# Kernel optimization log

Measured on AMD Instinct MI355X. Metric: run time of the kernel, lower is better.

The kernel has to match this reference:

```python
import jax, jax.numpy as jnp
import numpy as np


def _graph_conv(feat_src, e_src, e_dst, n_src, n_dst, W, b):
    # DGL GraphConv, norm='both', bipartite block; feat_src: [N_src, A, C, H]
    ones_e = jnp.ones(e_src.shape[0], dtype=feat_src.dtype)
    out_deg = jax.ops.segment_sum(ones_e, e_src, num_segments=n_src)
    in_deg = jax.ops.segment_sum(ones_e, e_dst, num_segments=n_dst)
    norm_src = jnp.clip(out_deg, 1.0) ** -0.5
    norm_dst = jnp.clip(in_deg, 1.0) ** -0.5
    feat = feat_src * norm_src[:, None, None, None]
    # in_feats == out_feats -> DGL multiplies by W before aggregation
    feat = jnp.einsum('nach,ho->naco', feat, W)
    msgs = feat[e_src]                                   # gather  [E, A, C, H]
    agg = jax.ops.segment_sum(msgs, e_dst, num_segments=n_dst)  # scatter-add
    return agg * norm_dst[:, None, None, None] + b


def setup_inputs() -> dict:
    key = jax.random.key(0)
    ks = jax.random.split(key, 8)
    H = 128
    N_SRC0, N_DST0, N_DST1 = 50000, 20000, 4096
    E0, E1 = 320000, 65536
    return {
        'in_feat': jax.random.normal(ks[0], (2, H, 2, N_SRC0), dtype=jnp.float32),
        'W': jax.random.normal(ks[1], (H, H), dtype=jnp.float32) / np.sqrt(H),
        'b': jnp.zeros((H,), dtype=jnp.float32),
        'e0_src': jax.random.randint(ks[2], (E0,), 0, N_SRC0, dtype=jnp.int32),
        'e0_dst': jax.random.randint(ks[3], (E0,), 0, N_DST0, dtype=jnp.int32),
        'e1_src': jax.random.randint(ks[4], (E1,), 0, N_DST0, dtype=jnp.int32),
        'e1_dst': jax.random.randint(ks[5], (E1,), 0, N_DST1, dtype=jnp.int32),
        'n_dst0': N_DST0,
        'n_dst1': N_DST1,
    }


def reference(in_feat, W, b, e0_src, e0_dst, e1_src, e1_dst, n_dst0, n_dst1):
    # [A, H, C, N] -> [N, A, C, H]
    x = jnp.transpose(in_feat, (3, 0, 2, 1))
    n_src0 = x.shape[0]
    h = _graph_conv(x, e0_src, e0_dst, n_src0, n_dst0, W, b)
    h = jax.nn.relu(h)
    h = _graph_conv(h, e1_src, e1_dst, n_dst0, n_dst1, W, b)
    h = jax.nn.relu(h)
    # [N_dst1, A, C, H] -> [A, H, C, N_dst1]
    out = jnp.transpose(h, (1, 3, 2, 0))
    return jax.nn.relu(out)
```

## Files before the change

kernel.cpp:

```cpp
#include <hip/hip_runtime.h>
#include <math.h>

#define H128 128
#define NF 512
typedef unsigned short u16;
typedef __attribute__((ext_vector_type(8))) short short8;
typedef __attribute__((ext_vector_type(4))) float floatx4;

__device__ inline u16 f2bf(float f) {
  union { float f; unsigned u; } x; x.f = f;
  unsigned r = x.u + 0x7FFFu + ((x.u >> 16) & 1u);
  return (u16)(r >> 16);
}
__device__ inline void addbf8(float* a, uint4 u) {
  a[0] += __uint_as_float(u.x << 16);
  a[1] += __uint_as_float(u.x & 0xFFFF0000u);
  a[2] += __uint_as_float(u.y << 16);
  a[3] += __uint_as_float(u.y & 0xFFFF0000u);
  a[4] += __uint_as_float(u.z << 16);
  a[5] += __uint_as_float(u.z & 0xFFFF0000u);
  a[6] += __uint_as_float(u.w << 16);
  a[7] += __uint_as_float(u.w & 0xFFFF0000u);
}

__global__ void k_count4(const int* __restrict__ e0s, const int* __restrict__ e0d,
                         const int* __restrict__ e1s, const int* __restrict__ e1d,
                         int E0, int E1,
                         int* __restrict__ c_s0, int* __restrict__ c_d0,
                         int* __restrict__ c_s1, int* __restrict__ c_d1) {
  int i = blockIdx.x * 256 + threadIdx.x;
  if (i < E0) { atomicAdd(&c_s0[e0s[i]], 1); return; }
  i -= E0;
  if (i < E0) { atomicAdd(&c_d0[e0d[i]], 1); return; }
  i -= E0;
  if (i < E1) { atomicAdd(&c_s1[e1s[i]], 1); return; }
  i -= E1;
  if (i < E1) { atomicAdd(&c_d1[e1d[i]], 1); }
}

__global__ void k_norm(int* __restrict__ buf, int n) {
  int i = blockIdx.x * 256 + threadIdx.x;
  if (i < n) {
    int d = buf[i];
    float dv = (d < 1) ? 1.0f : (float)d;
    ((float*)buf)[i] = 1.0f / sqrtf(dv);
  }
}

__global__ void k_scan2(const int* __restrict__ degA, int nA, int* __restrict__ offA, int* __restrict__ curA,
                        const int* __restrict__ degB, int nB, int* __restrict__ offB, int* __restrict__ curB) {
  const int* deg = blockIdx.x ? degB : degA;
  int n = blockIdx.x ? nB : nA;
  int* off = blockIdx.x ? offB : offA;
  int* cur = blockIdx.x ? curB : curA;
  __shared__ int wsum[16];
  const int tid = threadIdx.x;
  const int lane = tid & 63;
  const int wv = tid >> 6;
  const int per = (n + 1023) >> 10;
  const int base = tid * per;
  int cnt = n - base;
  if (cnt < 0) cnt = 0;
  if (cnt > per) cnt = per;
  int sum = 0;
  for (int i = 0; i < cnt; ++i) sum += deg[base + i];
  int x = sum;
  #pragma unroll
  for (int d2 = 1; d2 < 64; d2 <<= 1) {
    int y = __shfl_up(x, (unsigned)d2, 64);
    if (lane >= d2) x += y;
  }
  if (lane == 63) wsum[wv] = x;
  __syncthreads();
  if (wv == 0 && lane < 16) {
    int w = wsum[lane];
    #pragma unroll
    for (int d2 = 1; d2 < 16; d2 <<= 1) {
      int y = __shfl_up(w, (unsigned)d2, 64);
      if (lane >= d2) w += y;
    }
    wsum[lane] = w;
  }
  __syncthreads();
  int tbase = x - sum + (wv ? wsum[wv - 1] : 0);
  int running = tbase;
  for (int i = 0; i < cnt; ++i) {
    off[base + i] = running;
    cur[base + i] = running;
    running += deg[base + i];
  }
  if (tid == 1023) off[n] = wsum[15];
}

__global__ void k_scatter2(const int* __restrict__ e0s, const int* __restrict__ e0d,
                           const int* __restrict__ e1s, const int* __restrict__ e1d,
                           int E0, int E1,
                           int* __restrict__ cur0, int* __restrict__ csr0,
                           int* __restrict__ cur1, int* __restrict__ csr1) {
  int i = blockIdx.x * 256 + threadIdx.x;
  if (i < E0) {
    int p = atomicAdd(&cur0[e0d[i]], 1);
    csr0[p] = e0s[i];
    return;
  }
  i -= E0;
  if (i < E1) {
    int p = atomicAdd(&cur1[e1d[i]], 1);
    csr1[p] = e1s[i];
  }
}

__global__ void k_wfrag(const float* __restrict__ W, uint4* __restrict__ wfrag) {
  int t = blockIdx.x * 256 + threadIdx.x;
  int lane = t & 63;
  int pair = t >> 6;
  int ct = pair >> 2, kc = pair & 3;
  int quad = lane >> 4, r = lane & 15;
  const float* src = W + (size_t)(kc * 32 + quad * 8) * 128 + ct * 16 + r;
  union { u16 v[8]; uint4 u; } pk;
  #pragma unroll
  for (int j = 0; j < 8; ++j) pk.v[j] = f2bf(src[(size_t)j * 128]);
  wfrag[t] = pk.u;
}

__global__ __launch_bounds__(256) void k_transpose_in(
    const float* __restrict__ in, const float* __restrict__ norm,
    u16* __restrict__ xp, int N) {
  __shared__ float tile[64 * 128];
  const int tid = threadIdx.x;
  const int n0 = blockIdx.x << 6;
  const int ac = blockIdx.y;
  const int a = ac >> 1, c = ac & 1;
  const float* base = in + ((size_t)a * 256 + c) * (size_t)N;
  #pragma unroll
  for (int i = 0; i < 8; ++i) {
    int fidx = (i << 8) + tid;
    int h = fidx >> 4;
    int t = fidx & 15;
    int n = t << 2;
    int gn = n0 + n;
    float4 v = make_float4(0.f, 0.f, 0.f, 0.f);
    if (gn < N) v = *(const float4*)(base + (size_t)h * 2 * N + gn);
    int q = h >> 2, rem = h & 3;
    int rot = ((q + t) & 31) << 2;
    tile[(n + 0) * 128 + rot + rem] = v.x;
    tile[(n + 1) * 128 + rot + rem] = v.y;
    tile[(n + 2) * 128 + rot + rem] = v.z;
    tile[(n + 3) * 128 + rot + rem] = v.w;
  }
  __syncthreads();
  #pragma unroll
  for (int i = 0; i < 8; ++i) {
    int fidx = (i << 8) + tid;
    int h4 = fidx & 31;
    int n = fidx >> 5;
    int gn = n0 + n;
    if (gn < N) {
      float4 v = *(const float4*)(&tile[n * 128 + (((h4 + (n >> 2)) & 31) << 2)]);
      float s = norm[gn];
      ushort4 o;
      o.x = f2bf(v.x * s); o.y = f2bf(v.y * s);
      o.z = f2bf(v.z * s); o.w = f2bf(v.w * s);
      *(ushort4*)(xp + (size_t)gn * NF + ac * H128 + (h4 << 2)) = o;
    }
  }
}

__global__ __launch_bounds__(256) void k_agg(
    const u16* __restrict__ xp, const int* __restrict__ csr,
    const int* __restrict__ off, const float* __restrict__ norm_dst,
    u16* __restrict__ outp, int ndst) {
  const int wave = threadIdx.x >> 6;
  const int lane = threadIdx.x & 63;
  const int d = blockIdx.x * 4 + wave;
  if (d >= ndst) return;
  const int s = off[d], e = off[d + 1];
  float acc[8];
  #pragma unroll
  for (int i = 0; i < 8; ++i) acc[i] = 0.f;
  int j = s;
  for (; j + 4 <= e; j += 4) {
    int s0 = csr[j], s1 = csr[j + 1], s2 = csr[j + 2], s3 = csr[j + 3];
    uint4 u0 = *((const uint4*)(xp + (size_t)s0 * NF) + lane);
    uint4 u1 = *((const uint4*)(xp + (size_t)s1 * NF) + lane);
    uint4 u2 = *((const uint4*)(xp + (size_t)s2 * NF) + lane);
    uint4 u3 = *((const uint4*)(xp + (size_t)s3 * NF) + lane);
    addbf8(acc, u0); addbf8(acc, u1); addbf8(acc, u2); addbf8(acc, u3);
  }
  for (; j < e; ++j) {
    uint4 u = *((const uint4*)(xp + (size_t)csr[j] * NF) + lane);
    addbf8(acc, u);
  }
  float nd = norm_dst[d];
  u16* orow = outp + (size_t)d * NF + lane * 8;
  ushort4 o0, o1;
  o0.x = f2bf(acc[0] * nd); o0.y = f2bf(acc[1] * nd);
  o0.z = f2bf(acc[2] * nd); o0.w = f2bf(acc[3] * nd);
  o1.x = f2bf(acc[4] * nd); o1.y = f2bf(acc[5] * nd);
  o1.z = f2bf(acc[6] * nd); o1.w = f2bf(acc[7] * nd);
  *(ushort4*)orow = o0;
  *(ushort4*)(orow + 4) = o1;
}

template <bool OUT_BF16>
__global__ __launch_bounds__(256) void k_gemm_mfma(
    const u16* __restrict__ A, const uint4* __restrict__ wfrag,
    const float* __restrict__ bias, const float* __restrict__ scale,
    void* __restrict__ outv, int M) {
  __shared__ uint4 wb[2048];
  const int tid = threadIdx.x;
  #pragma unroll
  for (int i = 0; i < 8; ++i) wb[i * 256 + tid] = wfrag[i * 256 + tid];
  __syncthreads();
  const int wave = tid >> 6;
  const int lane = tid & 63;
  const int quad = lane >> 4;
  const int r = lane & 15;
  const int row0 = (blockIdx.x * 4 + wave) << 4;
  if (row0 >= M) return;
  short8 a[4];
  const u16* abase = A + (size_t)(row0 + r) * 128 + quad * 8;
  #pragma unroll
  for (int kc = 0; kc < 4; ++kc) a[kc] = *(const short8*)(abase + kc * 32);
  floatx4 acc[8];
  #pragma unroll
  for (int ct = 0; ct < 8; ++ct) acc[ct] = (floatx4){0.f, 0.f, 0.f, 0.f};
  #pragma unroll
  for (int kc = 0; kc < 4; ++kc) {
    #pragma unroll
    for (int ct = 0; ct < 8; ++ct) {
      short8 b = *(const short8*)&wb[(ct * 4 + kc) * 64 + lane];
      acc[ct] = __builtin_amdgcn_mfma_f32_16x16x32_bf16(a[kc], b, acc[ct], 0, 0, 0);
    }
  }
  float sc = scale ? scale[(row0 >> 2) + quad] : 1.f;
  #pragma unroll
  for (int ct = 0; ct < 8; ++ct) {
    float bcol = bias[ct * 16 + r];
    #pragma unroll
    for (int reg = 0; reg < 4; ++reg) {
      float v = acc[ct][reg] + bcol;
      v = (v > 0.f ? v : 0.f) * sc;
      size_t idx = (size_t)(row0 + quad * 4 + reg) * 128 + ct * 16 + r;
      if (OUT_BF16) ((u16*)outv)[idx] = f2bf(v);
      else          ((float*)outv)[idx] = v;
    }
  }
}

__global__ __launch_bounds__(256) void k_transpose_out(
    const float* __restrict__ h1, float* __restrict__ out, int N) {
  __shared__ float tile[128][68];
  const int tid = threadIdx.x;
  const int n0 = blockIdx.x << 6;
  const int ac = blockIdx.y;
  const int a = ac >> 1, c = ac & 1;
  #pragma unroll
  for (int i = 0; i < 8; ++i) {
    int fidx = (i << 8) + tid;
    int h4 = fidx & 31;
    int n = fidx >> 5;
    float4 v = *(const float4*)(h1 + (size_t)(n0 + n) * NF + ac * H128 + (h4 << 2));
    int h = h4 << 2;
    tile[h + 0][n] = v.x; tile[h + 1][n] = v.y;
    tile[h + 2][n] = v.z; tile[h + 3][n] = v.w;
  }
  __syncthreads();
  float* obase = out + ((size_t)a * 256 + c) * (size_t)N;
  #pragma unroll
  for (int i = 0; i < 8; ++i) {
    int fidx = (i << 8) + tid;
    int h = fidx >> 4;
    int n = (fidx & 15) << 2;
    float4 v = *(const float4*)(&tile[h][n]);
    *(float4*)(obase + (size_t)h * 2 * N + n0 + n) = v;
  }
}

extern "C" void kernel_launch(void* const* d_in, const int* in_sizes, int n_in,
                              void* d_out, int out_size, void* d_ws, size_t ws_size,
                              hipStream_t stream) {
  const float* in_feat = (const float*)d_in[0];
  const float* W       = (const float*)d_in[1];
  const float* bias    = (const float*)d_in[2];
  const int* e0_src    = (const int*)d_in[3];
  const int* e0_dst    = (const int*)d_in[4];
  const int* e1_src    = (const int*)d_in[5];
  const int* e1_dst    = (const int*)d_in[6];
  const int N_DST0 = 20000;
  const int N_DST1 = 4096;
  const int N_SRC0 = in_sizes[0] / NF;
  const int E0 = in_sizes[3];
  const int E1 = in_sizes[5];

  u16* xp    = (u16*)d_ws;
  u16* h0    = xp + (size_t)N_SRC0 * NF;
  u16* agg0b = h0 + (size_t)N_DST0 * NF;
  u16* agg1b = agg0b + (size_t)N_DST0 * NF;
  float* h1  = (float*)(agg1b + (size_t)N_DST1 * NF);
  int* ibase    = (int*)(h1 + (size_t)N_DST1 * NF);
  int* cnt_src0 = ibase;
  int* cnt_dst0 = cnt_src0 + N_SRC0;
  int* cnt_src1 = cnt_dst0 + N_DST0;
  int* cnt_dst1 = cnt_src1 + N_DST0;
  int* off0 = cnt_dst1 + N_DST1;
  int* cur0 = off0 + N_DST0 + 1;
  int* csr0 = cur0 + N_DST0;
  int* off1 = csr0 + E0;
  int* cur1 = off1 + N_DST1 + 1;
  int* csr1 = cur1 + N_DST1;
  uint4* wfrag = (uint4*)(((uintptr_t)(csr1 + E1) + 15) & ~(uintptr_t)15);

  const int NCNT = N_SRC0 + N_DST0 + N_DST0 + N_DST1;
  hipMemsetAsync(cnt_src0, 0, (size_t)NCNT * sizeof(int), stream);

  int tot_cnt = 2 * E0 + 2 * E1;
  k_count4<<<(tot_cnt + 255) / 256, 256, 0, stream>>>(
      e0_src, e0_dst, e1_src, e1_dst, E0, E1, cnt_src0, cnt_dst0, cnt_src1, cnt_dst1);

  k_scan2<<<2, 1024, 0, stream>>>(cnt_dst0, N_DST0, off0, cur0,
                                  cnt_dst1, N_DST1, off1, cur1);

  k_norm<<<(NCNT + 255) / 256, 256, 0, stream>>>(cnt_src0, NCNT);

  k_scatter2<<<(E0 + E1 + 255) / 256, 256, 0, stream>>>(
      e0_src, e0_dst, e1_src, e1_dst, E0, E1, cur0, csr0, cur1, csr1);

  k_wfrag<<<8, 256, 0, stream>>>(W, wfrag);

  dim3 tg1((N_SRC0 + 63) / 64, 4);
  k_transpose_in<<<tg1, 256, 0, stream>>>(in_feat, (const float*)cnt_src0, xp, N_SRC0);

  k_agg<<<(N_DST0 + 3) / 4, 256, 0, stream>>>(
      xp, csr0, off0, (const float*)cnt_dst0, agg0b, N_DST0);
  k_gemm_mfma<true><<<(N_DST0 * 4) / 64, 256, 0, stream>>>(
      agg0b, wfrag, bias, (const float*)cnt_src1, (void*)h0, N_DST0 * 4);

  k_agg<<<(N_DST1 + 3) / 4, 256, 0, stream>>>(
      h0, csr1, off1, (const float*)cnt_dst1, agg1b, N_DST1);
  k_gemm_mfma<false><<<(N_DST1 * 4) / 64, 256, 0, stream>>>(
      agg1b, wfrag, bias, nullptr, (void*)h1, N_DST1 * 4);

  dim3 tg2(N_DST1 / 64, 4);
  k_transpose_out<<<tg2, 256, 0, stream>>>(h1, (float*)d_out, N_DST1);
}
```

Baseline: 354.8 us.

## Merge preprocessing kernels and fuse CSR scatter with input transpose

Folds count4 into a two-atomic-per-thread count kernel, merges scan, norm and weight-fragment conversion into one multi-role prep kernel, and runs the CSR scatter in the same launch as the input transpose by partitioning blocks. Degree norms now go to a separate float buffer so the scan and the norm computation can run concurrently. The aggregation loop is unrolled to 8 outstanding gathers to raise memory-level parallelism. Together these cut the number of launches and the serialization between small kernels, at the cost of role-divergent blocks and a larger transpose block size.

Result: faster. 338.8 us (-4.5%).

```diff
diff --git a/kernel.cpp b/kernel.cpp
--- a/kernel.cpp
+++ b/kernel.cpp
@@ -23,118 +23,130 @@
   a[7] += __uint_as_float(u.w & 0xFFFF0000u);
 }
 
-__global__ void k_count4(const int* __restrict__ e0s, const int* __restrict__ e0d,
+__global__ void k_count2(const int* __restrict__ e0s, const int* __restrict__ e0d,
                          const int* __restrict__ e1s, const int* __restrict__ e1d,
                          int E0, int E1,
                          int* __restrict__ c_s0, int* __restrict__ c_d0,
                          int* __restrict__ c_s1, int* __restrict__ c_d1) {
   int i = blockIdx.x * 256 + threadIdx.x;
-  if (i < E0) { atomicAdd(&c_s0[e0s[i]], 1); return; }
-  i -= E0;
-  if (i < E0) { atomicAdd(&c_d0[e0d[i]], 1); return; }
-  i -= E0;
-  if (i < E1) { atomicAdd(&c_s1[e1s[i]], 1); return; }
-  i -= E1;
-  if (i < E1) { atomicAdd(&c_d1[e1d[i]], 1); }
-}
-
-__global__ void k_norm(int* __restrict__ buf, int n) {
-  int i = blockIdx.x * 256 + threadIdx.x;
-  if (i < n) {
-    int d = buf[i];
-    float dv = (d < 1) ? 1.0f : (float)d;
-    ((float*)buf)[i] = 1.0f / sqrtf(dv);
-  }
-}
-
-__global__ void k_scan2(const int* __restrict__ degA, int nA, int* __restrict__ offA, int* __restrict__ curA,
-                        const int* __restrict__ degB, int nB, int* __restrict__ offB, int* __restrict__ curB) {
-  const int* deg = blockIdx.x ? degB : degA;
-  int n = blockIdx.x ? nB : nA;
-  int* off = blockIdx.x ? offB : offA;
-  int* cur = blockIdx.x ? curB : curA;
-  __shared__ int wsum[16];
-  const int tid = threadIdx.x;
-  const int lane = tid & 63;
-  const int wv = tid >> 6;
-  const int per = (n + 1023) >> 10;
-  const int base = tid * per;
-  int cnt = n - base;
-  if (cnt < 0) cnt = 0;
-  if (cnt > per) cnt = per;
-  int sum = 0;
-  for (int i = 0; i < cnt; ++i) sum += deg[base + i];
-  int x = sum;
-  #pragma unroll
-  for (int d2 = 1; d2 < 64; d2 <<= 1) {
-    int y = __shfl_up(x, (unsigned)d2, 64);
-    if (lane >= d2) x += y;
-  }
-  if (lane == 63) wsum[wv] = x;
-  __syncthreads();
-  if (wv == 0 && lane < 16) {
-    int w = wsum[lane];
-    #pragma unroll
-    for (int d2 = 1; d2 < 16; d2 <<= 1) {
-      int y = __shfl_up(w, (unsigned)d2, 64);
-      if (lane >= d2) w += y;
-    }
-    wsum[lane] = w;
-  }
-  __syncthreads();
-  int tbase = x - sum + (wv ? wsum[wv - 1] : 0);
-  int running = tbase;
-  for (int i = 0; i < cnt; ++i) {
-    off[base + i] = running;
-    cur[base + i] = running;
-    running += deg[base + i];
-  }
-  if (tid == 1023) off[n] = wsum[15];
-}
-
-__global__ void k_scatter2(const int* __restrict__ e0s, const int* __restrict__ e0d,
-                           const int* __restrict__ e1s, const int* __restrict__ e1d,
-                           int E0, int E1,
-                           int* __restrict__ cur0, int* __restrict__ csr0,
-                           int* __restrict__ cur1, int* __restrict__ csr1) {
-  int i = blockIdx.x * 256 + threadIdx.x;
   if (i < E0) {
-    int p = atomicAdd(&cur0[e0d[i]], 1);
-    csr0[p] = e0s[i];
+    atomicAdd(&c_s0[e0s[i]], 1);
+    atomicAdd(&c_d0[e0d[i]], 1);
     return;
   }
   i -= E0;
   if (i < E1) {
-    int p = atomicAdd(&cur1[e1d[i]], 1);
-    csr1[p] = e1s[i];
-  }
-}
-
-__global__ void k_wfrag(const float* __restrict__ W, uint4* __restrict__ wfrag) {
-  int t = blockIdx.x * 256 + threadIdx.x;
-  int lane = t & 63;
-  int pair = t >> 6;
-  int ct = pair >> 2, kc = pair & 3;
-  int quad = lane >> 4, r = lane & 15;
-  const float* src = W + (size_t)(kc * 32 + quad * 8) * 128 + ct * 16 + r;
-  union { u16 v[8]; uint4 u; } pk;
-  #pragma unroll
-  for (int j = 0; j < 8; ++j) pk.v[j] = f2bf(src[(size_t)j * 128]);
-  wfrag[t] = pk.u;
-}
-
-__global__ __launch_bounds__(256) void k_transpose_in(
+    atomicAdd(&c_s1[e1s[i]], 1);
+    atomicAdd(&c_d1[e1d[i]], 1);
+  }
+}
+
+__global__ __launch_bounds__(1024) void k_prep(
+    const int* __restrict__ cnt, int NCNT, float* __restrict__ normf,
+    const int* __restrict__ degA, int nA, int* __restrict__ offA, int* __restrict__ curA,
+    const int* __restrict__ degB, int nB, int* __restrict__ offB, int* __restrict__ curB,
+    const float* __restrict__ W, uint4* __restrict__ wfrag) {
+  __shared__ int wsum[16];
+  const int b = blockIdx.x;
+  const int tid = threadIdx.x;
+  if (b < 2) {
+    const int* deg = b ? degB : degA;
+    int n = b ? nB : nA;
+    int* off = b ? offB : offA;
+    int* cur = b ? curB : curA;
+    const int lane = tid & 63;
+    const int wv = tid >> 6;
+    const int per = (n + 1023) >> 10;
+    const int base = tid * per;
+    int cntk = n - base;
+    if (cntk < 0) cntk = 0;
+    if (cntk > per) cntk = per;
+    int sum = 0;
+    for (int i = 0; i < cntk; ++i) sum += deg[base + i];
+    int x = sum;
+    #pragma unroll
+    for (int d2 = 1; d2 < 64; d2 <<= 1) {
+      int y = __shfl_up(x, (unsigned)d2, 64);
+      if (lane >= d2) x += y;
+    }
+    if (lane == 63) wsum[wv] = x;
+    __syncthreads();
+    if (wv == 0 && lane < 16) {
+      int w = wsum[lane];
+      #pragma unroll
+      for (int d2 = 1; d2 < 16; d2 <<= 1) {
+        int y = __shfl_up(w, (unsigned)d2, 64);
+        if (lane >= d2) w += y;
+      }
+      wsum[lane] = w;
+    }
+    __syncthreads();
+    int tbase = x - sum + (wv ? wsum[wv - 1] : 0);
+    int running = tbase;
+    for (int i = 0; i < cntk; ++i) {
+      off[base + i] = running;
+      cur[base + i] = running;
+      running += deg[base + i];
+    }
+    if (tid == 1023) off[n] = wsum[15];
+    return;
+  }
+  if (b < 4) {
+    int t = (b - 2) * 1024 + tid;
+    if (t < 2048) {
+      int lane = t & 63;
+      int pair = t >> 6;
+      int ct = pair >> 2, kc = pair & 3;
+      int quad = lane >> 4, r = lane & 15;
+      const float* src = W + (size_t)(kc * 32 + quad * 8) * 128 + ct * 16 + r;
+      union { u16 v[8]; uint4 u; } pk;
+      #pragma unroll
+      for (int j = 0; j < 8; ++j) pk.v[j] = f2bf(src[(size_t)j * 128]);
+      wfrag[t] = pk.u;
+    }
+    return;
+  }
+  int i = (b - 4) * 1024 + tid;
+  if (i < NCNT) {
+    int d = cnt[i];
+    float dv = (d < 1) ? 1.0f : (float)d;
+    normf[i] = 1.0f / sqrtf(dv);
+  }
+}
+
+__global__ __launch_bounds__(512) void k_tin_scatter(
     const float* __restrict__ in, const float* __restrict__ norm,
-    u16* __restrict__ xp, int N) {
+    u16* __restrict__ xp, int N, int SB,
+    const int* __restrict__ e0s, const int* __restrict__ e0d,
+    const int* __restrict__ e1s, const int* __restrict__ e1d,
+    int E0, int E1,
+    int* __restrict__ cur0, int* __restrict__ csr0,
+    int* __restrict__ cur1, int* __restrict__ csr1) {
   __shared__ float tile[64 * 128];
+  const int bid = blockIdx.x;
   const int tid = threadIdx.x;
-  const int n0 = blockIdx.x << 6;
-  const int ac = blockIdx.y;
+  if (bid < SB) {
+    int i = bid * 512 + tid;
+    if (i < E0) {
+      int p = atomicAdd(&cur0[e0d[i]], 1);
+      csr0[p] = e0s[i];
+      return;
+    }
+    i -= E0;
+    if (i < E1) {
+      int p = atomicAdd(&cur1[e1d[i]], 1);
+      csr1[p] = e1s[i];
+    }
+    return;
+  }
+  const int tb = bid - SB;
+  const int n0 = (tb >> 2) << 6;
+  const int ac = tb & 3;
   const int a = ac >> 1, c = ac & 1;
   const float* base = in + ((size_t)a * 256 + c) * (size_t)N;
   #pragma unroll
-  for (int i = 0; i < 8; ++i) {
-    int fidx = (i << 8) + tid;
+  for (int i = 0; i < 4; ++i) {
+    int fidx = (i << 9) + tid;
     int h = fidx >> 4;
     int t = fidx & 15;
     int n = t << 2;
@@ -150,8 +162,8 @@
   }
   __syncthreads();
   #pragma unroll
-  for (int i = 0; i < 8; ++i) {
-    int fidx = (i << 8) + tid;
+  for (int i = 0; i < 4; ++i) {
+    int fidx = (i << 9) + tid;
     int h4 = fidx & 31;
     int n = fidx >> 5;
     int gn = n0 + n;
@@ -175,22 +187,26 @@
   const int d = blockIdx.x * 4 + wave;
   if (d >= ndst) return;
   const int s = off[d], e = off[d + 1];
+  const uint4* xpl = (const uint4*)xp + lane;
   float acc[8];
   #pragma unroll
   for (int i = 0; i < 8; ++i) acc[i] = 0.f;
   int j = s;
+  for (; j + 8 <= e; j += 8) {
+    uint4 u[8];
+    #pragma unroll
+    for (int k = 0; k < 8; ++k) u[k] = xpl[(size_t)csr[j + k] * 64];
+    #pragma unroll
+    for (int k = 0; k < 8; ++k) addbf8(acc, u[k]);
+  }
   for (; j + 4 <= e; j += 4) {
-    int s0 = csr[j], s1 = csr[j + 1], s2 = csr[j + 2], s3 = csr[j + 3];
-    uint4 u0 = *((const uint4*)(xp + (size_t)s0 * NF) + lane);
-    uint4 u1 = *((const uint4*)(xp + (size_t)s1 * NF) + lane);
-    uint4 u2 = *((const uint4*)(xp + (size_t)s2 * NF) + lane);
-    uint4 u3 = *((const uint4*)(xp + (size_t)s3 * NF) + lane);
-    addbf8(acc, u0); addbf8(acc, u1); addbf8(acc, u2); addbf8(acc, u3);
-  }
-  for (; j < e; ++j) {
-    uint4 u = *((const uint4*)(xp + (size_t)csr[j] * NF) + lane);
-    addbf8(acc, u);
-  }
+    uint4 u[4];
+    #pragma unroll
+    for (int k = 0; k < 4; ++k) u[k] = xpl[(size_t)csr[j + k] * 64];
+    #pragma unroll
+    for (int k = 0; k < 4; ++k) addbf8(acc, u[k]);
+  }
+  for (; j < e; ++j) addbf8(acc, xpl[(size_t)csr[j] * 64]);
   float nd = norm_dst[d];
   u16* orow = outp + (size_t)d * NF + lane * 8;
   ushort4 o0, o1;
@@ -310,34 +326,38 @@
   int* cur1 = off1 + N_DST1 + 1;
   int* csr1 = cur1 + N_DST1;
   uint4* wfrag = (uint4*)(((uintptr_t)(csr1 + E1) + 15) & ~(uintptr_t)15);
+  float* normf = (float*)(wfrag + 2048);
+  float* normf_src0 = normf;
+  float* normf_dst0 = normf_src0 + N_SRC0;
+  float* normf_src1 = normf_dst0 + N_DST0;
+  float* normf_dst1 = normf_src1 + N_DST0;
 
   const int NCNT = N_SRC0 + N_DST0 + N_DST0 + N_DST1;
   hipMemsetAsync(cnt_src0, 0, (size_t)NCNT * sizeof(int), stream);
 
-  int tot_cnt = 2 * E0 + 2 * E1;
-  k_count4<<<(tot_cnt + 255) / 256, 256, 0, stream>>>(
+  k_count2<<<(E0 + E1 + 255) / 256, 256, 0, stream>>>(
       e0_src, e0_dst, e1_src, e1_dst, E0, E1, cnt_src0, cnt_dst0, cnt_src1, cnt_dst1);
 
-  k_scan2<<<2, 1024, 0, stream>>>(cnt_dst0, N_DST0, off0, cur0,
-                                  cnt_dst1, N_DST1, off1, cur1);
-
-  k_norm<<<(NCNT + 255) / 256, 256, 0, stream>>>(cnt_src0, NCNT);
-
-  k_scatter2<<<(E0 + E1 + 255) / 256, 256, 0, stream>>>(
-      e0_src, e0_dst, e1_src, e1_dst, E0, E1, cur0, csr0, cur1, csr1);
-
-  k_wfrag<<<8, 256, 0, stream>>>(W, wfrag);
-
-  dim3 tg1((N_SRC0 + 63) / 64, 4);
-  k_transpose_in<<<tg1, 256, 0, stream>>>(in_feat, (const float*)cnt_src0, xp, N_SRC0);
+  k_prep<<<4 + (NCNT + 1023) / 1024, 1024, 0, stream>>>(
+      cnt_src0, NCNT, normf,
+      cnt_dst0, N_DST0, off0, cur0,
+      cnt_dst1, N_DST1, off1, cur1,
+      W, wfrag);
+
+  const int SB = (E0 + E1 + 511) / 512;
+  const int TB = ((N_SRC0 + 63) / 64) * 4;
+  k_tin_scatter<<<SB + TB, 512, 0, stream>>>(
+      in_feat, normf_src0, xp, N_SRC0, SB,
+      e0_src, e0_dst, e1_src, e1_dst, E0, E1,
+      cur0, csr0, cur1, csr1);
 
   k_agg<<<(N_DST0 + 3) / 4, 256, 0, stream>>>(
-      xp, csr0, off0, (const float*)cnt_dst0, agg0b, N_DST0);
+      xp, csr0, off0, normf_dst0, agg0b, N_DST0);
   k_gemm_mfma<true><<<(N_DST0 * 4) / 64, 256, 0, stream>>>(
-      agg0b, wfrag, bias, (const float*)cnt_src1, (void*)h0, N_DST0 * 4);
+      agg0b, wfrag, bias, normf_src1, (void*)h0, N_DST0 * 4);
 
   k_agg<<<(N_DST1 + 3) / 4, 256, 0, stream>>>(
-      h0, csr1, off1, (const float*)cnt_dst1, agg1b, N_DST1);
+      h0, csr1, off1, normf_dst1, agg1b, N_DST1);
   k_gemm_mfma<false><<<(N_DST1 * 4) / 64, 256, 0, stream>>>(
       agg1b, wfrag, bias, nullptr, (void*)h1, N_DST1 * 4);
 
```
